# Performance work log

Measured on AMD Instinct MI355X. Metric: run time of the kernel, lower is better.

Reference implementation:

```python
import jax, jax.numpy as jnp
import numpy as np

MARGIN = 1.0


def setup_inputs() -> dict:
    key = jax.random.key(0)
    k1, k2, k3 = jax.random.split(key, 3)
    N, F = 4096, 512
    a = jax.random.normal(k1, (N, F), dtype=jnp.float32)
    b = jax.random.normal(k2, (N, F), dtype=jnp.float32)
    labels = jax.random.randint(k3, (N,), 0, 16, dtype=jnp.int32)
    return {"a": a, "b": b, "labels": labels}


def reference(a, b, labels):
    # D[i, j] = ||b_i - a_j||  (torch: Xa=a[None], Xb=b[:,None], sum over feat)
    # GEMM form of the pairwise sqdist; clamp tiny fp negatives before sqrt.
    Dsq = (jnp.sum(b * b, axis=1)[:, None]
           + jnp.sum(a * a, axis=1)[None, :]
           - 2.0 * (b @ a.T))
    D = jnp.sqrt(jnp.maximum(Dsq, 0.0))            # [N, N]
    Dexpm = jnp.exp(MARGIN - D)                    # [N, N]

    same = labels[:, None] == labels[None, :]      # [N, N]
    eye = jnp.eye(labels.shape[0], dtype=bool)
    pos_mask = same & ~eye                         # ordered positive pairs (i, j)
    neg_mask = ~same                               # negative pairs (labels differ)

    # neg_i sum for row i: sum_k Dexpm[i, k] over k with labels[k] != labels[i]
    row_negsum = jnp.sum(jnp.where(neg_mask, Dexpm, 0.0), axis=1)  # [N]

    # J_ij = log(neg_ik_sum + neg_jl_sum) + D[i, j]; hinged and squared
    J = jnp.log(row_negsum[:, None] + row_negsum[None, :]) + D
    hinge_sq = jnp.square(jnp.maximum(J, 0.0))

    num_pos = jnp.sum(pos_mask)
    return jnp.sum(jnp.where(pos_mask, hinge_sq, 0.0)) / (2.0 * num_pos)
```

## Files before the change

kernel.cpp:

```cpp
#include <hip/hip_runtime.h>
#include <math.h>

#define NROW 4096
#define FDIM 512
#define MARGIN 1.0f
#define NLAB 16
#define PREP_BLK 512

typedef __attribute__((ext_vector_type(8))) short short8;
typedef __attribute__((ext_vector_type(4))) float floatx4;

__device__ inline unsigned short f2bf(float x) {
    unsigned u = __float_as_uint(x);
    return (unsigned short)((u + 0x7FFFu + ((u >> 16) & 1u)) >> 16);
}
__device__ inline void glds16(const unsigned short* g, unsigned short* l) {
    __builtin_amdgcn_global_load_lds(
        (const __attribute__((address_space(1))) unsigned int*)g,
        (__attribute__((address_space(3))) unsigned int*)l, 16, 0, 0);
}

__global__ __launch_bounds__(256) void prep_kernel(
    const float* __restrict__ a, const float* __restrict__ b,
    const int* __restrict__ labels,
    unsigned short* __restrict__ abf, unsigned short* __restrict__ bbf,
    float* __restrict__ na, float* __restrict__ nb,
    float* __restrict__ rns, float* __restrict__ loss,
    int* __restrict__ perm, int* __restrict__ goff,
    int* __restrict__ wl, int* __restrict__ wlmeta) {
    const int t = threadIdx.x;

    if (blockIdx.x == PREP_BLK) {
        __shared__ int hist[NLAB], off[NLAB], cur[NLAB];
        if (t < NLAB) hist[t] = 0;
        __syncthreads();
        for (int i = t; i < NROW; i += 256) atomicAdd(&hist[labels[i] & 15], 1);
        __syncthreads();
        if (t == 0) {
            int acc = 0;
            for (int g = 0; g < NLAB; ++g) { off[g] = acc; acc += hist[g]; }
            int n = 0;
            long long np = 0;
            for (int g = 0; g < NLAB; ++g) {
                goff[g] = off[g];
                int c = hist[g];
                np += (long long)c * (long long)(c - 1);
                int nt = (c + 63) >> 6;
                for (int ti = 0; ti < nt; ++ti)
                    for (int tj = 0; tj < nt; ++tj)
                        wl[n++] = (g << 12) | (ti << 6) | tj;
            }
            goff[NLAB] = NROW;
            wlmeta[0] = n;
            wlmeta[1] = (int)np;
            wlmeta[2] = 0;
            loss[0]   = 0.f;
        }
        __syncthreads();
        if (t < NLAB) cur[t] = off[t];
        __syncthreads();
        for (int i = t; i < NROW; i += 256) {
            int pos = atomicAdd(&cur[labels[i] & 15], 1);
            perm[pos] = i;
        }
        return;
    }

    const int grp = t >> 5;
    const int ln  = t & 31;
    const int row = blockIdx.x * 8 + grp;
    const float4* a4 = (const float4*)(a + (size_t)row * FDIM);
    const float4* b4 = (const float4*)(b + (size_t)row * FDIM);
    float sa = 0.f, sb = 0.f;
    #pragma unroll
    for (int k = 0; k < 2; ++k) {
        int f = ln * 2 + k * 64;
        float4 va0 = a4[f], va1 = a4[f + 1];
        float4 vb0 = b4[f], vb1 = b4[f + 1];
        sa += va0.x * va0.x + va0.y * va0.y + va0.z * va0.z + va0.w * va0.w
            + va1.x * va1.x + va1.y * va1.y + va1.z * va1.z + va1.w * va1.w;
        sb += vb0.x * vb0.x + vb0.y * vb0.y + vb0.z * vb0.z + vb0.w * vb0.w
            + vb1.x * vb1.x + vb1.y * vb1.y + vb1.z * vb1.z + vb1.w * vb1.w;
        short8 ua, ub;
        ua[0] = (short)f2bf(va0.x); ua[1] = (short)f2bf(va0.y);
        ua[2] = (short)f2bf(va0.z); ua[3] = (short)f2bf(va0.w);
        ua[4] = (short)f2bf(va1.x); ua[5] = (short)f2bf(va1.y);
        ua[6] = (short)f2bf(va1.z); ua[7] = (short)f2bf(va1.w);
        ub[0] = (short)f2bf(vb0.x); ub[1] = (short)f2bf(vb0.y);
        ub[2] = (short)f2bf(vb0.z); ub[3] = (short)f2bf(vb0.w);
        ub[4] = (short)f2bf(vb1.x); ub[5] = (short)f2bf(vb1.y);
        ub[6] = (short)f2bf(vb1.z); ub[7] = (short)f2bf(vb1.w);
        *(short8*)&abf[(size_t)row * FDIM + (size_t)f * 4] = ua;
        *(short8*)&bbf[(size_t)row * FDIM + (size_t)f * 4] = ub;
    }
    #pragma unroll
    for (int o = 16; o > 0; o >>= 1) {
        sa += __shfl_down(sa, o, 32);
        sb += __shfl_down(sb, o, 32);
    }
    if (ln == 0) {
        na[row] = sa;
        nb[row] = sb;
        rns[row] = 0.f;
    }
}

__global__ __launch_bounds__(256) void pass_neg(
    const unsigned short* __restrict__ abf, const unsigned short* __restrict__ bbf,
    const int* __restrict__ labels,
    const float* __restrict__ na, const float* __restrict__ nb,
    float* __restrict__ rns)
{
    __shared__ __align__(16) unsigned short arena[16384];
    __shared__ int   li_s[128], lj_s[128];
    __shared__ float nb_s[128], na_s[128];

    const int t    = threadIdx.x;
    const int lane = t & 63;
    const int w    = t >> 6;
    const int wi   = w >> 1, wj = w & 1;
    const int bid  = blockIdx.x;
    const int sup  = bid >> 6, loc = bid & 63;
    const int by   = ((sup >> 2) << 3) | (loc >> 3);
    const int bx   = ((sup & 3) << 3) | (loc & 7);
    const int ti   = by * 128;
    const int tj   = bx * 128;
    const int lr   = lane & 15;
    const int lq   = lane >> 4;
    const int qe   = lq ^ ((lr >> 1) & 3);

    floatx4 acc[4][4];
    #pragma unroll
    for (int i = 0; i < 4; ++i)
        #pragma unroll
        for (int j = 0; j < 4; ++j)
            acc[i][j] = (floatx4){0.f, 0.f, 0.f, 0.f};

    if (t < 128) {
        li_s[t] = labels[ti + t];
        nb_s[t] = nb[ti + t];
    } else {
        int u = t - 128;
        lj_s[u] = labels[tj + u];
        na_s[u] = na[tj + u];
    }

    auto stage = [&](int kk, int buf) {
        unsigned short* As = arena + buf * 8192;
        unsigned short* Bs = arena + 4096 + buf * 8192;
        #pragma unroll
        for (int l = 0; l < 2; ++l) {
            int c   = t + l * 256;
            int row = c >> 2;
            int q   = c & 3;
            int qs  = q ^ ((row >> 1) & 3);
            glds16(abf + (size_t)(tj + row) * FDIM + kk + qs * 8, As + c * 8);
            glds16(bbf + (size_t)(ti + row) * FDIM + kk + qs * 8, Bs + c * 8);
        }
    };

    stage(0, 0);
    __syncthreads();

    #pragma unroll
    for (int it = 0; it < FDIM / 32; ++it) {
        if (it < FDIM / 32 - 1) stage((it + 1) * 32, (it + 1) & 1);

        const unsigned short* As = arena + (it & 1) * 8192;
        const unsigned short* Bs = As + 4096;
        short8 af[4], bf[4];
        #pragma unroll
        for (int ri = 0; ri < 4; ++ri)
            af[ri] = *(const short8*)&Bs[(wi * 64 + ri * 16 + lr) * 32 + qe * 8];
        #pragma unroll
        for (int rj = 0; rj < 4; ++rj)
            bf[rj] = *(const short8*)&As[(wj * 64 + rj * 16 + lr) * 32 + qe * 8];
        #pragma unroll
        for (int ri = 0; ri < 4; ++ri)
            #pragma unroll
            for (int rj = 0; rj < 4; ++rj)
                acc[ri][rj] = __builtin_amdgcn_mfma_f32_16x16x32_bf16(
                    af[ri], bf[rj], acc[ri][rj], 0, 0, 0);
        __syncthreads();
    }

    #pragma unroll
    for (int ri = 0; ri < 4; ++ri) {
        float rs[4] = {0.f, 0.f, 0.f, 0.f};
        #pragma unroll
        for (int rj = 0; rj < 4; ++rj) {
            int   jl  = wj * 64 + rj * 16 + lr;
            float naj = na_s[jl];
            int   ljv = lj_s[jl];
            #pragma unroll
            for (int r = 0; r < 4; ++r) {
                int il = wi * 64 + ri * 16 + lq * 4 + r;
                if (li_s[il] != ljv) {
                    float dsq = nb_s[il] + naj - 2.f * acc[ri][rj][r];
                    float D   = sqrtf(fmaxf(dsq, 0.f));
                    rs[r] += __expf(MARGIN - D);
                }
            }
        }
        #pragma unroll
        for (int r = 0; r < 4; ++r) {
            #pragma unroll
            for (int o = 8; o > 0; o >>= 1) rs[r] += __shfl_down(rs[r], o, 16);
        }
        if (lr == 0) {
            #pragma unroll
            for (int r = 0; r < 4; ++r)
                atomicAdd(&rns[ti + wi * 64 + ri * 16 + lq * 4 + r], rs[r]);
        }
    }
}

__global__ __launch_bounds__(256) void pass2_pos(
    const unsigned short* __restrict__ abf, const unsigned short* __restrict__ bbf,
    const float* __restrict__ na, const float* __restrict__ nb,
    const float* __restrict__ rns,
    const int* __restrict__ perm, const int* __restrict__ goff,
    const int* __restrict__ wl, const int* __restrict__ wlmeta,
    float* __restrict__ loss_sum, int* __restrict__ done,
    float* __restrict__ out)
{
    __shared__ __align__(16) unsigned short arena[16384];
    __shared__ int   rows_i[64], rows_j[64];
    __shared__ float rbi_s[64], rbj_s[64], nbi_s[64], naj_s[64];
    __shared__ float part[4];

    const int t    = threadIdx.x;
    const int lane = t & 63;
    const int w    = t >> 6;
    const int wi   = w >> 1, wj = w & 1;
    const int lr   = lane & 15;
    const int lq   = lane >> 4;
    const int nwl  = wlmeta[0];

    float local = 0.f;

    for (int item = blockIdx.x; item < nwl; item += gridDim.x) {
        __syncthreads();
        int e  = wl[item];
        int g  = e >> 12, ti = (e >> 6) & 63, tj = e & 63;
        int gb = goff[g], ge = goff[g + 1];
        int cnt = ge - gb;

        if (t < 64) {
            int idx = gb + ti * 64 + t;
            int ig  = perm[idx < ge ? idx : gb];
            rows_i[t] = ig;
            rbi_s[t]  = rns[ig];
            nbi_s[t]  = nb[ig];
        } else if (t < 128) {
            int u   = t - 64;
            int idx = gb + tj * 64 + u;
            int jg  = perm[idx < ge ? idx : gb];
            rows_j[u] = jg;
            rbj_s[u]  = rns[jg];
            naj_s[u]  = na[jg];
        }
        __syncthreads();

        floatx4 acc[2][2];
        #pragma unroll
        for (int i = 0; i < 2; ++i)
            #pragma unroll
            for (int j = 0; j < 2; ++j)
                acc[i][j] = (floatx4){0.f, 0.f, 0.f, 0.f};

        auto stage = [&](int kk) {
            #pragma unroll
            for (int l = 0; l < 4; ++l) {
                int c   = t + l * 256;
                int row = c >> 4;
                int qs  = (c & 15) ^ (row & 7);
                glds16(abf + (size_t)rows_j[row] * FDIM + kk + qs * 8,
                       arena + c * 8);
                glds16(bbf + (size_t)rows_i[row] * FDIM + kk + qs * 8,
                       arena + 8192 + c * 8);
            }
        };

        stage(0);
        __syncthreads();

        #pragma unroll
        for (int itk = 0; itk < 4; ++itk) {
            const unsigned short* As = arena;
            const unsigned short* Bs = arena + 8192;
            #pragma unroll
            for (int ks = 0; ks < 4; ++ks) {
                short8 af[2], bfv[2];
                #pragma unroll
                for (int ri = 0; ri < 2; ++ri) {
                    int R = wi * 32 + ri * 16 + lr;
                    af[ri] = *(const short8*)
                        &Bs[R * 128 + (((ks * 4 + lq) ^ (R & 7))) * 8];
                }
                #pragma unroll
                for (int rj = 0; rj < 2; ++rj) {
                    int R = wj * 32 + rj * 16 + lr;
                    bfv[rj] = *(const short8*)
                        &As[R * 128 + (((ks * 4 + lq) ^ (R & 7))) * 8];
                }
                #pragma unroll
                for (int ri = 0; ri < 2; ++ri)
                    #pragma unroll
                    for (int rj = 0; rj < 2; ++rj)
                        acc[ri][rj] = __builtin_amdgcn_mfma_f32_16x16x32_bf16(
                            af[ri], bfv[rj], acc[ri][rj], 0, 0, 0);
            }
            if (itk < 3) {
                __syncthreads();
                stage((itk + 1) * 128);
                __syncthreads();
            }
        }

        #pragma unroll
        for (int ri = 0; ri < 2; ++ri)
            #pragma unroll
            for (int rj = 0; rj < 2; ++rj) {
                int  jl  = wj * 32 + rj * 16 + lr;
                bool vj  = (tj * 64 + jl) < cnt;
                int  jg  = rows_j[jl];
                float nav = naj_s[jl], rbj = rbj_s[jl];
                #pragma unroll
                for (int r = 0; r < 4; ++r) {
                    int  il = wi * 32 + ri * 16 + lq * 4 + r;
                    bool vi = (ti * 64 + il) < cnt;
                    if (vi && vj && rows_i[il] != jg) {
                        float dsq = nbi_s[il] + nav - 2.f * acc[ri][rj][r];
                        float D   = sqrtf(fmaxf(dsq, 0.f));
                        float J   = __logf(rbi_s[il] + rbj) + D;
                        float h   = fmaxf(J, 0.f);
                        local += h * h;
                    }
                }
            }
    }

    #pragma unroll
    for (int o = 32; o > 0; o >>= 1) local += __shfl_down(local, o);
    if (lane == 0) part[w] = local;
    __syncthreads();
    if (t == 0) {
        atomicAdd(loss_sum, part[0] + part[1] + part[2] + part[3]);
        __threadfence();
        int old = atomicAdd(done, 1);
        if (old == (int)gridDim.x - 1) {
            __threadfence();
            float total = *(volatile float*)loss_sum;
            out[0] = total / (2.0f * (float)wlmeta[1]);
        }
    }
}

extern "C" void kernel_launch(void* const* d_in, const int* in_sizes, int n_in,
                              void* d_out, int out_size, void* d_ws, size_t ws_size,
                              hipStream_t stream) {
    const float* a      = (const float*)d_in[0];
    const float* b      = (const float*)d_in[1];
    const int*   labels = (const int*)d_in[2];
    float* out = (float*)d_out;

    unsigned short* abf = (unsigned short*)d_ws;
    unsigned short* bbf = abf + (size_t)NROW * FDIM;
    float* fws  = (float*)(bbf + (size_t)NROW * FDIM);
    float* na   = fws;
    float* nb   = fws + NROW;
    float* rns  = fws + 2 * NROW;
    float* loss = fws + 3 * NROW;
    int* iws    = (int*)(fws + 3 * NROW + 4);
    int* perm   = iws;
    int* goff   = iws + NROW;
    int* wlmeta = iws + NROW + 20;
    int* wl     = iws + NROW + 24;

    prep_kernel<<<PREP_BLK + 1, 256, 0, stream>>>(a, b, labels, abf, bbf,
                                                  na, nb, rns, loss,
                                                  perm, goff, wl, wlmeta);
    pass_neg<<<(NROW / 128) * (NROW / 128), 256, 0, stream>>>(abf, bbf, labels,
                                                              na, nb, rns);
    pass2_pos<<<384, 256, 0, stream>>>(abf, bbf, na, nb, rns, perm, goff, wl,
                                       wlmeta, loss, &wlmeta[2], out);
}
```

Measured before the change: 141.6 us.

## Enlarge pass_neg tiles to 256x256 with 512 threads and reduce row sums in LDS

The negative-sum GEMM pass moves from 128x128 tiles with 4 waves to 256x256 tiles with 8 waves, a K step of 64, and a new XOR swizzle. Per-wave row partials are now combined in shared memory before one atomic per row, which cuts global atomics. The larger tiles give more reuse per loaded byte, but use 128KB of LDS and more accumulator registers, and launch only 256 blocks. The prep kernel now uses one wave per row, and pass2 block count changes.

```diff
diff --git a/kernel.cpp b/kernel.cpp
--- a/kernel.cpp
+++ b/kernel.cpp
@@ -5,7 +5,7 @@
 #define FDIM 512
 #define MARGIN 1.0f
 #define NLAB 16
-#define PREP_BLK 512
+#define PREP_BLK 1024
 
 typedef __attribute__((ext_vector_type(8))) short short8;
 typedef __attribute__((ext_vector_type(4))) float floatx4;
@@ -66,37 +66,33 @@
         return;
     }
 
-    const int grp = t >> 5;
-    const int ln  = t & 31;
-    const int row = blockIdx.x * 8 + grp;
+    const int grp = t >> 6;
+    const int ln  = t & 63;
+    const int row = blockIdx.x * 4 + grp;
     const float4* a4 = (const float4*)(a + (size_t)row * FDIM);
     const float4* b4 = (const float4*)(b + (size_t)row * FDIM);
-    float sa = 0.f, sb = 0.f;
-    #pragma unroll
-    for (int k = 0; k < 2; ++k) {
-        int f = ln * 2 + k * 64;
-        float4 va0 = a4[f], va1 = a4[f + 1];
-        float4 vb0 = b4[f], vb1 = b4[f + 1];
-        sa += va0.x * va0.x + va0.y * va0.y + va0.z * va0.z + va0.w * va0.w
-            + va1.x * va1.x + va1.y * va1.y + va1.z * va1.z + va1.w * va1.w;
-        sb += vb0.x * vb0.x + vb0.y * vb0.y + vb0.z * vb0.z + vb0.w * vb0.w
-            + vb1.x * vb1.x + vb1.y * vb1.y + vb1.z * vb1.z + vb1.w * vb1.w;
-        short8 ua, ub;
-        ua[0] = (short)f2bf(va0.x); ua[1] = (short)f2bf(va0.y);
-        ua[2] = (short)f2bf(va0.z); ua[3] = (short)f2bf(va0.w);
-        ua[4] = (short)f2bf(va1.x); ua[5] = (short)f2bf(va1.y);
-        ua[6] = (short)f2bf(va1.z); ua[7] = (short)f2bf(va1.w);
-        ub[0] = (short)f2bf(vb0.x); ub[1] = (short)f2bf(vb0.y);
-        ub[2] = (short)f2bf(vb0.z); ub[3] = (short)f2bf(vb0.w);
-        ub[4] = (short)f2bf(vb1.x); ub[5] = (short)f2bf(vb1.y);
-        ub[6] = (short)f2bf(vb1.z); ub[7] = (short)f2bf(vb1.w);
-        *(short8*)&abf[(size_t)row * FDIM + (size_t)f * 4] = ua;
-        *(short8*)&bbf[(size_t)row * FDIM + (size_t)f * 4] = ub;
-    }
-    #pragma unroll
-    for (int o = 16; o > 0; o >>= 1) {
-        sa += __shfl_down(sa, o, 32);
-        sb += __shfl_down(sb, o, 32);
+    const int f = ln * 2;
+    float4 va0 = a4[f], va1 = a4[f + 1];
+    float4 vb0 = b4[f], vb1 = b4[f + 1];
+    float sa = va0.x * va0.x + va0.y * va0.y + va0.z * va0.z + va0.w * va0.w
+             + va1.x * va1.x + va1.y * va1.y + va1.z * va1.z + va1.w * va1.w;
+    float sb = vb0.x * vb0.x + vb0.y * vb0.y + vb0.z * vb0.z + vb0.w * vb0.w
+             + vb1.x * vb1.x + vb1.y * vb1.y + vb1.z * vb1.z + vb1.w * vb1.w;
+    short8 ua, ub;
+    ua[0] = (short)f2bf(va0.x); ua[1] = (short)f2bf(va0.y);
+    ua[2] = (short)f2bf(va0.z); ua[3] = (short)f2bf(va0.w);
+    ua[4] = (short)f2bf(va1.x); ua[5] = (short)f2bf(va1.y);
+    ua[6] = (short)f2bf(va1.z); ua[7] = (short)f2bf(va1.w);
+    ub[0] = (short)f2bf(vb0.x); ub[1] = (short)f2bf(vb0.y);
+    ub[2] = (short)f2bf(vb0.z); ub[3] = (short)f2bf(vb0.w);
+    ub[4] = (short)f2bf(vb1.x); ub[5] = (short)f2bf(vb1.y);
+    ub[6] = (short)f2bf(vb1.z); ub[7] = (short)f2bf(vb1.w);
+    *(short8*)&abf[(size_t)row * FDIM + (size_t)f * 4] = ua;
+    *(short8*)&bbf[(size_t)row * FDIM + (size_t)f * 4] = ub;
+    #pragma unroll
+    for (int o = 32; o > 0; o >>= 1) {
+        sa += __shfl_down(sa, o);
+        sb += __shfl_down(sb, o);
     }
     if (ln == 0) {
         na[row] = sa;
@@ -105,55 +101,44 @@
     }
 }
 
-__global__ __launch_bounds__(256) void pass_neg(
+__global__ __launch_bounds__(512, 2) void pass_neg(
     const unsigned short* __restrict__ abf, const unsigned short* __restrict__ bbf,
     const int* __restrict__ labels,
     const float* __restrict__ na, const float* __restrict__ nb,
     float* __restrict__ rns)
 {
-    __shared__ __align__(16) unsigned short arena[16384];
-    __shared__ int   li_s[128], lj_s[128];
-    __shared__ float nb_s[128], na_s[128];
+    __shared__ __align__(16) unsigned short arena[65536];
+    __shared__ float rpart[4][256];
 
     const int t    = threadIdx.x;
     const int lane = t & 63;
     const int w    = t >> 6;
-    const int wi   = w >> 1, wj = w & 1;
-    const int bid  = blockIdx.x;
-    const int sup  = bid >> 6, loc = bid & 63;
-    const int by   = ((sup >> 2) << 3) | (loc >> 3);
-    const int bx   = ((sup & 3) << 3) | (loc & 7);
-    const int ti   = by * 128;
-    const int tj   = bx * 128;
+    const int wi   = w >> 2;
+    const int wj   = w & 3;
     const int lr   = lane & 15;
     const int lq   = lane >> 4;
-    const int qe   = lq ^ ((lr >> 1) & 3);
-
-    floatx4 acc[4][4];
-    #pragma unroll
-    for (int i = 0; i < 4; ++i)
+
+    const int bid = blockIdx.x;
+    const int wg  = (bid & 7) * 32 + (bid >> 3);
+    const int by  = wg >> 4, bx = wg & 15;
+    const int ti  = by * 256;
+    const int tj  = bx * 256;
+
+    floatx4 acc[8][4];
+    #pragma unroll
+    for (int i = 0; i < 8; ++i)
         #pragma unroll
         for (int j = 0; j < 4; ++j)
             acc[i][j] = (floatx4){0.f, 0.f, 0.f, 0.f};
 
-    if (t < 128) {
-        li_s[t] = labels[ti + t];
-        nb_s[t] = nb[ti + t];
-    } else {
-        int u = t - 128;
-        lj_s[u] = labels[tj + u];
-        na_s[u] = na[tj + u];
-    }
-
     auto stage = [&](int kk, int buf) {
-        unsigned short* As = arena + buf * 8192;
-        unsigned short* Bs = arena + 4096 + buf * 8192;
-        #pragma unroll
-        for (int l = 0; l < 2; ++l) {
-            int c   = t + l * 256;
-            int row = c >> 2;
-            int q   = c & 3;
-            int qs  = q ^ ((row >> 1) & 3);
+        unsigned short* As = arena + buf * 32768;
+        unsigned short* Bs = As + 16384;
+        #pragma unroll
+        for (int l = 0; l < 4; ++l) {
+            int c   = t + l * 512;
+            int row = c >> 3;
+            int qs  = (c & 7) ^ (row & 7);
             glds16(abf + (size_t)(tj + row) * FDIM + kk + qs * 8, As + c * 8);
             glds16(bbf + (size_t)(ti + row) * FDIM + kk + qs * 8, Bs + c * 8);
         }
@@ -162,46 +147,63 @@
     stage(0, 0);
     __syncthreads();
 
-    #pragma unroll
-    for (int it = 0; it < FDIM / 32; ++it) {
-        if (it < FDIM / 32 - 1) stage((it + 1) * 32, (it + 1) & 1);
-
-        const unsigned short* As = arena + (it & 1) * 8192;
-        const unsigned short* Bs = As + 4096;
-        short8 af[4], bf[4];
-        #pragma unroll
-        for (int ri = 0; ri < 4; ++ri)
-            af[ri] = *(const short8*)&Bs[(wi * 64 + ri * 16 + lr) * 32 + qe * 8];
+    for (int it = 0; it < FDIM / 64; ++it) {
+        if (it < FDIM / 64 - 1) stage((it + 1) * 64, (it + 1) & 1);
+
+        const unsigned short* As = arena + (it & 1) * 32768;
+        const unsigned short* Bs = As + 16384;
+        #pragma unroll
+        for (int s = 0; s < 2; ++s) {
+            short8 af[8], bv[4];
+            #pragma unroll
+            for (int ri = 0; ri < 8; ++ri) {
+                int R = wi * 128 + ri * 16 + lr;
+                af[ri] = *(const short8*)
+                    &Bs[R * 64 + (((s * 4 + lq) ^ (R & 7))) * 8];
+            }
+            #pragma unroll
+            for (int rj = 0; rj < 4; ++rj) {
+                int R = wj * 64 + rj * 16 + lr;
+                bv[rj] = *(const short8*)
+                    &As[R * 64 + (((s * 4 + lq) ^ (R & 7))) * 8];
+            }
+            #pragma unroll
+            for (int ri = 0; ri < 8; ++ri)
+                #pragma unroll
+                for (int rj = 0; rj < 4; ++rj)
+                    acc[ri][rj] = __builtin_amdgcn_mfma_f32_16x16x32_bf16(
+                        af[ri], bv[rj], acc[ri][rj], 0, 0, 0);
+        }
+        __syncthreads();
+    }
+
+    int   ljv[4]; float najv[4];
+    #pragma unroll
+    for (int rj = 0; rj < 4; ++rj) {
+        int jl = wj * 64 + rj * 16 + lr;
+        ljv[rj]  = labels[tj + jl];
+        najv[rj] = na[tj + jl];
+    }
+    #pragma unroll
+    for (int ri = 0; ri < 8; ++ri) {
+        float rs[4] = {0.f, 0.f, 0.f, 0.f};
+        int liv[4]; float nbv[4];
+        #pragma unroll
+        for (int r = 0; r < 4; ++r) {
+            int il = wi * 128 + ri * 16 + lq * 4 + r;
+            liv[r] = labels[ti + il];
+            nbv[r] = nb[ti + il];
+        }
         #pragma unroll
         for (int rj = 0; rj < 4; ++rj)
-            bf[rj] = *(const short8*)&As[(wj * 64 + rj * 16 + lr) * 32 + qe * 8];
-        #pragma unroll
-        for (int ri = 0; ri < 4; ++ri)
-            #pragma unroll
-            for (int rj = 0; rj < 4; ++rj)
-                acc[ri][rj] = __builtin_amdgcn_mfma_f32_16x16x32_bf16(
-                    af[ri], bf[rj], acc[ri][rj], 0, 0, 0);
-        __syncthreads();
-    }
-
-    #pragma unroll
-    for (int ri = 0; ri < 4; ++ri) {
-        float rs[4] = {0.f, 0.f, 0.f, 0.f};
-        #pragma unroll
-        for (int rj = 0; rj < 4; ++rj) {
-            int   jl  = wj * 64 + rj * 16 + lr;
-            float naj = na_s[jl];
-            int   ljv = lj_s[jl];
             #pragma unroll
             for (int r = 0; r < 4; ++r) {
-                int il = wi * 64 + ri * 16 + lq * 4 + r;
-                if (li_s[il] != ljv) {
-                    float dsq = nb_s[il] + naj - 2.f * acc[ri][rj][r];
+                if (liv[r] != ljv[rj]) {
+                    float dsq = nbv[r] + najv[rj] - 2.f * acc[ri][rj][r];
                     float D   = sqrtf(fmaxf(dsq, 0.f));
                     rs[r] += __expf(MARGIN - D);
                 }
             }
-        }
         #pragma unroll
         for (int r = 0; r < 4; ++r) {
             #pragma unroll
@@ -210,8 +212,13 @@
         if (lr == 0) {
             #pragma unroll
             for (int r = 0; r < 4; ++r)
-                atomicAdd(&rns[ti + wi * 64 + ri * 16 + lq * 4 + r], rs[r]);
-        }
+                rpart[wj][wi * 128 + ri * 16 + lq * 4 + r] = rs[r];
+        }
+    }
+    __syncthreads();
+    if (t < 256) {
+        float s = rpart[0][t] + rpart[1][t] + rpart[2][t] + rpart[3][t];
+        atomicAdd(&rns[ti + t], s);
     }
 }
 
@@ -381,8 +388,8 @@
     prep_kernel<<<PREP_BLK + 1, 256, 0, stream>>>(a, b, labels, abf, bbf,
                                                   na, nb, rns, loss,
                                                   perm, goff, wl, wlmeta);
-    pass_neg<<<(NROW / 128) * (NROW / 128), 256, 0, stream>>>(abf, bbf, labels,
+    pass_neg<<<(NROW / 256) * (NROW / 256), 512, 0, stream>>>(abf, bbf, labels,
                                                               na, nb, rns);
-    pass2_pos<<<384, 256, 0, stream>>>(abf, bbf, na, nb, rns, perm, goff, wl,
+    pass2_pos<<<256, 256, 0, stream>>>(abf, bbf, na, nb, rns, perm, goff, wl,
                                        wlmeta, loss, &wlmeta[2], out);
 }
```

Measured after the change: 135.9 us. 1.04x faster.
